# Optimization experiments

Hardware: AMD Instinct MI355X
Metric: run time of the kernel (lower is better)

The kernel has to match this reference:

```python
import jax, jax.numpy as jnp
import numpy as np
from jax import lax

H = 128      # hidden_size
KK = 4       # num_kernels (TemporalConv k)
NL = 2       # rgcn num_layers
C = 32       # convtranse channels
KS = 3       # convtranse kernel_size
NE = 40000   # num_ents
NR = 256     # num_rels
T = 4        # history length
E = 100000   # edges per snapshot
NT = 1024    # num query triplets


def _norm(x):
    return x / jnp.maximum(jnp.linalg.norm(x, axis=-1, keepdims=True), 1e-12)


def _gru(x, h, wih, whh, bih, bhh):
    gi = x @ wih.T + bih
    gh = h @ whh.T + bhh
    ir, iz, inn = jnp.split(gi, 3, axis=-1)
    hr, hz, hn = jnp.split(gh, 3, axis=-1)
    r = jax.nn.sigmoid(ir + hr)
    z = jax.nn.sigmoid(iz + hz)
    n = jnp.tanh(inn + r * hn)
    return (1.0 - z) * n + z * h


def _tconv(e, t, w, b, pw, pb):
    # e: (N,H), t: (1,H) -> kernels (KK,1,H//KK)
    v = (t @ w.T + b).reshape(KK, 1, -1)
    f = lax.conv_general_dilated(e[:, None, :], v, (1,), 'VALID',
                                 dimension_numbers=('NCH', 'OIH', 'NCH'))  # (N,KK,H-H//KK+1)
    return f.reshape(f.shape[0], -1) @ pw.T + pb


def _convtranse(x, ck, cb, fw, fb):
    p = KS // 2
    y = lax.conv_general_dilated(x, ck, (1,), [(p, p)],
                                 dimension_numbers=('NCH', 'OIH', 'NCH')) + cb[None, :, None]
    y = jax.nn.relu(y)
    return jax.nn.relu(y.reshape(y.shape[0], -1) @ fw.T + fb)


def _agg_rel(nf, s, d, r):
    # dense (num_rels, num_nodes) bool mask via scatter, then per-rel mean of touched nodes
    mask = jnp.zeros((NR, NE), bool).at[r, s].set(True).at[r, d].set(True)
    m = mask.astype(nf.dtype)
    su = m @ nf
    c = m.sum(1, keepdims=True)
    return jnp.where(c > 0, su / jnp.maximum(c, 1.0), 0.0)


def _rgcn(h, ef, s, d, wn, ws, b):
    ones = jnp.ones((s.shape[0], 1), h.dtype)
    for l in range(NL):
        msg = h[s] + ef
        sums = jax.ops.segment_sum(msg, d, num_segments=NE)
        cnt = jax.ops.segment_sum(ones, d, num_segments=NE)
        agg = sums / jnp.maximum(cnt, 1.0)
        h = jax.nn.relu(agg @ wn[l] + h @ ws[l] + b[l])
    return h


def setup_inputs() -> dict:
    key = jax.random.key(0)
    ks = jax.random.split(key, 40)
    f32 = jnp.float32
    pin = H * KK - H + KK  # TemporalConv pooling in-features
    inp = {
        'ent_embeds': jax.random.normal(ks[0], (NE, H), f32),
        'rel_embeds': jax.random.normal(ks[1], (NR, H), f32) * 0.1,
        'mmt_embed': jax.random.normal(ks[2], (1, H), f32) * 0.1,
        'tc_w': jax.random.normal(ks[3], (H, H), f32) * 0.05,
        'tc_b': jnp.zeros((H,), f32),
        'tc_pw': jax.random.normal(ks[4], (H, pin), f32) * 0.05,
        'tc_pb': jnp.zeros((H,), f32),
        'gru1_wih': jax.random.normal(ks[5], (3 * H, 2 * H), f32) * 0.05,
        'gru1_whh': jax.random.normal(ks[6], (3 * H, H), f32) * 0.05,
        'gru1_bih': jnp.zeros((3 * H,), f32),
        'gru1_bhh': jnp.zeros((3 * H,), f32),
        'l1_wih': jax.random.normal(ks[7], (3 * H, H), f32) * 0.05,
        'l1_whh': jax.random.normal(ks[8], (3 * H, H), f32) * 0.05,
        'l1_bih': jnp.zeros((3 * H,), f32),
        'l1_bhh': jnp.zeros((3 * H,), f32),
        'l2_wih': jax.random.normal(ks[9], (3 * H, H), f32) * 0.05,
        'l2_whh': jax.random.normal(ks[10], (3 * H, H), f32) * 0.05,
        'l2_bih': jnp.zeros((3 * H,), f32),
        'l2_bhh': jnp.zeros((3 * H,), f32),
        'lin_w': jax.random.normal(ks[11], (H, H), f32) * 0.05,
        'lin_b': jnp.zeros((H,), f32),
        'rgcn_wn': jax.random.normal(ks[12], (NL, H, H), f32) * 0.05,
        'rgcn_ws': jax.random.normal(ks[13], (NL, H, H), f32) * 0.05,
        'rgcn_b': jnp.zeros((NL, H), f32),
        'oc_k': jax.random.normal(ks[14], (C, 2, KS), f32) * 0.1,
        'oc_kb': jnp.zeros((C,), f32),
        'oc_fw': jax.random.normal(ks[15], (H, C * H), f32) * 0.02,
        'oc_fb': jnp.zeros((H,), f32),
        'rc_k': jax.random.normal(ks[16], (C, 2, KS), f32) * 0.1,
        'rc_kb': jnp.zeros((C,), f32),
        'rc_fw': jax.random.normal(ks[17], (H, C * H), f32) * 0.02,
        'rc_fb': jnp.zeros((H,), f32),
        'src': jax.random.randint(ks[18], (T, E), 0, NE, jnp.int32),
        'dst': jax.random.randint(ks[19], (T, E), 0, NE, jnp.int32),
        'rid': jax.random.randint(ks[20], (T, E), 0, NR, jnp.int32),
        'subj': jax.random.randint(ks[21], (NT,), 0, NE, jnp.int32),
        'rel': jax.random.randint(ks[22], (NT,), 0, NR, jnp.int32),
        'obj': jax.random.randint(ks[23], (NT,), 0, NE, jnp.int32),
    }
    return inp


def reference(ent_embeds, rel_embeds, mmt_embed, tc_w, tc_b, tc_pw, tc_pb,
              gru1_wih, gru1_whh, gru1_bih, gru1_bhh,
              l1_wih, l1_whh, l1_bih, l1_bhh,
              l2_wih, l2_whh, l2_bih, l2_bhh,
              lin_w, lin_b, rgcn_wn, rgcn_ws, rgcn_b,
              oc_k, oc_kb, oc_fw, oc_fb, rc_k, rc_kb, rc_fw, rc_fb,
              src, dst, rid, subj, rel, obj):
    rel_param = rel_embeds  # the raw parameter, used inside the loop
    ent = _norm(ent_embeds)
    relh = _norm(rel_embeds)
    mmt = mmt_embed
    zero = jnp.zeros_like(mmt)
    for t in range(T):
        s, d, r = src[t], dst[t], rid[t]
        n_mmt = _gru(mmt, zero, l1_wih, l1_whh, l1_bih, l1_bhh)
        g = _gru(mmt, zero, l2_wih, l2_whh, l2_bih, l2_bhh)
        mmt = mmt + g * (n_mmt - mmt)
        ent = _tconv(ent, mmt, tc_w, tc_b, tc_pw, tc_pb)
        relh = _tconv(relh, mmt, tc_w, tc_b, tc_pw, tc_pb)
        rel_ent = _agg_rel(ent, s, d, r)
        gru_in = jnp.concatenate([rel_ent, rel_param], axis=-1)
        n_rel = _gru(gru_in, relh, gru1_wih, gru1_whh, gru1_bih, gru1_bhh)
        n_rel = _norm(n_rel)
        efeat = n_rel[r]
        nf = _rgcn(ent, efeat, s, d, rgcn_wn, rgcn_ws, rgcn_b)
        nf = _norm(nf)
        u = jax.nn.sigmoid(ent @ lin_w.T + lin_b)
        ent = ent + u * (nf - ent)
        relh = n_rel
    obj_pred = jnp.stack([ent[subj], relh[rel]], axis=1)    # (NT,2,H)
    obj_logit = _convtranse(obj_pred, oc_k, oc_kb, oc_fw, oc_fb) @ ent.T
    rel_pred = jnp.stack([ent[subj], ent[obj]], axis=1)
    rel_logit = _convtranse(rel_pred, rc_k, rc_kb, rc_fw, rc_fb) @ relh.T
    return obj_logit, rel_logit
```

## Files before the change

kernel.cpp:

```cpp
#include <hip/hip_runtime.h>
#include <cmath>


namespace {

constexpr int H   = 128;
constexpr int KK  = 4;
constexpr int C   = 32;
constexpr int NE  = 40000;
constexpr int NR  = 256;
constexpr int T   = 4;
constexpr int E   = 100000;
constexpr int NT  = 1024;
constexpr int PIN = 388;
constexpr int MW  = 1280;
constexpr int MWU = 1250;
constexpr size_t NEH = (size_t)NE * H;

__device__ __forceinline__ float sigm(float x) { return 1.0f / (1.0f + expf(-x)); }

__global__ __launch_bounds__(256) void norm_rows(const float* __restrict__ in,
                                                 float* __restrict__ out, int n) {
  int row  = blockIdx.x * 4 + (threadIdx.x >> 6);
  int lane = threadIdx.x & 63;
  if (row >= n) return;
  const float2* ip = reinterpret_cast<const float2*>(in + (size_t)row * H);
  float2 v = ip[lane];
  float ss = v.x * v.x + v.y * v.y;
#pragma unroll
  for (int off = 32; off; off >>= 1) ss += __shfl_xor(ss, off);
  float inv = 1.0f / fmaxf(sqrtf(ss), 1e-12f);
  float2 o; o.x = v.x * inv; o.y = v.y * inv;
  reinterpret_cast<float2*>(out + (size_t)row * H)[lane] = o;
}

__global__ void copy_vec(const float* __restrict__ a, float* __restrict__ b, int n) {
  int i = blockIdx.x * blockDim.x + threadIdx.x;
  if (i < n) b[i] = a[i];
}

__global__ __launch_bounds__(256) void transpose128(const float* __restrict__ in,
                                                    float* __restrict__ out) {
  int i = blockIdx.x * 256 + threadIdx.x;
  int o = i >> 7, k = i & 127;
  out[k * H + o] = in[o * H + k];
}

__global__ __launch_bounds__(128) void mmt_step(
    const float* __restrict__ mmt_in,
    const float* __restrict__ w1, const float* __restrict__ bi1, const float* __restrict__ bh1,
    const float* __restrict__ w2, const float* __restrict__ bi2, const float* __restrict__ bh2,
    const float* __restrict__ tcw, const float* __restrict__ tcb,
    float* __restrict__ mmt_out, float* __restrict__ vout) {
  __shared__ float sm[H], sm2[H];
  int t = threadIdx.x;
  sm[t] = mmt_in[t];
  __syncthreads();
  float g1r = bi1[t], g1z = bi1[H + t], g1n = bi1[2 * H + t];
  float g2r = bi2[t], g2z = bi2[H + t], g2n = bi2[2 * H + t];
  for (int k = 0; k < H; k++) {
    float x = sm[k];
    g1r += x * w1[t * H + k];
    g1z += x * w1[(H + t) * H + k];
    g1n += x * w1[(2 * H + t) * H + k];
    g2r += x * w2[t * H + k];
    g2z += x * w2[(H + t) * H + k];
    g2n += x * w2[(2 * H + t) * H + k];
  }
  float r1 = sigm(g1r + bh1[t]), z1 = sigm(g1z + bh1[H + t]);
  float n1 = tanhf(g1n + r1 * bh1[2 * H + t]);
  float nmmt = (1.0f - z1) * n1;
  float r2 = sigm(g2r + bh2[t]), z2 = sigm(g2z + bh2[H + t]);
  float n2 = tanhf(g2n + r2 * bh2[2 * H + t]);
  float gg = (1.0f - z2) * n2;
  float m  = sm[t];
  float mo = m + gg * (nmmt - m);
  mmt_out[t] = mo;
  sm2[t] = mo;
  __syncthreads();
  float v = tcb[t];
  for (int k = 0; k < H; k++) v += sm2[k] * tcw[t * H + k];
  vout[t] = v;
}

__global__ __launch_bounds__(128) void build_M(const float* __restrict__ v,
                                               const float* __restrict__ pw,
                                               float* __restrict__ MT) {
  int o = blockIdx.x, p = threadIdx.x;
  __shared__ float sp[PIN];
  __shared__ float sv[H];
  for (int i = p; i < PIN; i += H) sp[i] = pw[(size_t)o * PIN + i];
  sv[p] = v[p];
  __syncthreads();
  float acc = 0.0f;
  int jlo = p - 31 > 0 ? p - 31 : 0;
  int jhi = p < 96 ? p : 96;
#pragma unroll
  for (int k = 0; k < KK; k++)
    for (int j = jlo; j <= jhi; j++) acc += sp[k * 97 + j] * sv[k * 32 + (p - j)];
  MT[p * H + o] = acc;
}


__global__ __launch_bounds__(256) void gemm_bias(const float* __restrict__ X,
                                                 const float* __restrict__ WT,
                                                 const float* __restrict__ bias,
                                                 float* __restrict__ out) {
  __shared__ float sX[64 * H];
  int t = threadIdx.x;
  int base = blockIdx.x * 64;
  const float4* gx = reinterpret_cast<const float4*>(X + (size_t)base * H);
  float4* sx4 = reinterpret_cast<float4*>(sX);
#pragma unroll
  for (int i = 0; i < 8; i++) sx4[t + 256 * i] = gx[t + 256 * i];
  __syncthreads();
  int oq = (t & 31) * 4, ng = (t >> 5) * 8;
  float acc[8][4] = {};
  for (int k = 0; k < H; k += 4) {
    float4 w0 = *reinterpret_cast<const float4*>(&WT[(k + 0) * H + oq]);
    float4 w1 = *reinterpret_cast<const float4*>(&WT[(k + 1) * H + oq]);
    float4 w2 = *reinterpret_cast<const float4*>(&WT[(k + 2) * H + oq]);
    float4 w3 = *reinterpret_cast<const float4*>(&WT[(k + 3) * H + oq]);
#pragma unroll
    for (int m = 0; m < 8; m++) {
      float4 x = *reinterpret_cast<const float4*>(&sX[(ng + m) * H + k]);
      acc[m][0] += x.x * w0.x + x.y * w1.x + x.z * w2.x + x.w * w3.x;
      acc[m][1] += x.x * w0.y + x.y * w1.y + x.z * w2.y + x.w * w3.y;
      acc[m][2] += x.x * w0.z + x.y * w1.z + x.z * w2.z + x.w * w3.z;
      acc[m][3] += x.x * w0.w + x.y * w1.w + x.z * w2.w + x.w * w3.w;
    }
  }
  float4 b4 = *reinterpret_cast<const float4*>(&bias[oq]);
#pragma unroll
  for (int m = 0; m < 8; m++) {
    float4 o4 = {acc[m][0] + b4.x, acc[m][1] + b4.y, acc[m][2] + b4.z, acc[m][3] + b4.w};
    *reinterpret_cast<float4*>(&out[(size_t)(base + ng + m) * H + oq]) = o4;
  }
}

__global__ __launch_bounds__(256) void gemm_rgcn(const float* __restrict__ A,
                                                 const float* __restrict__ Hm,
                                                 const float* __restrict__ wn,
                                                 const float* __restrict__ ws,
                                                 const float* __restrict__ bias,
                                                 const int* __restrict__ deg,
                                                 float* __restrict__ out) {
  __shared__ float sA[32 * H];
  __shared__ float sH[32 * H];
  int t = threadIdx.x;
  int base = blockIdx.x * 32;
  const float4* ga = reinterpret_cast<const float4*>(A + (size_t)base * H);
  const float4* gh = reinterpret_cast<const float4*>(Hm + (size_t)base * H);
  float4* sa4 = reinterpret_cast<float4*>(sA);
  float4* sh4 = reinterpret_cast<float4*>(sH);
#pragma unroll
  for (int i = 0; i < 4; i++) { sa4[t + 256 * i] = ga[t + 256 * i]; sh4[t + 256 * i] = gh[t + 256 * i]; }
  __syncthreads();
  int oq = (t & 31) * 4, ng = (t >> 5) * 4;
  float accA[4][4] = {}, accS[4][4] = {};
  for (int k = 0; k < H; k += 4) {
    float4 n0 = *reinterpret_cast<const float4*>(&wn[(k + 0) * H + oq]);
    float4 n1 = *reinterpret_cast<const float4*>(&wn[(k + 1) * H + oq]);
    float4 n2 = *reinterpret_cast<const float4*>(&wn[(k + 2) * H + oq]);
    float4 n3 = *reinterpret_cast<const float4*>(&wn[(k + 3) * H + oq]);
    float4 s0 = *reinterpret_cast<const float4*>(&ws[(k + 0) * H + oq]);
    float4 s1 = *reinterpret_cast<const float4*>(&ws[(k + 1) * H + oq]);
    float4 s2 = *reinterpret_cast<const float4*>(&ws[(k + 2) * H + oq]);
    float4 s3 = *reinterpret_cast<const float4*>(&ws[(k + 3) * H + oq]);
#pragma unroll
    for (int m = 0; m < 4; m++) {
      float4 a = *reinterpret_cast<const float4*>(&sA[(ng + m) * H + k]);
      float4 h = *reinterpret_cast<const float4*>(&sH[(ng + m) * H + k]);
      accA[m][0] += a.x * n0.x + a.y * n1.x + a.z * n2.x + a.w * n3.x;
      accA[m][1] += a.x * n0.y + a.y * n1.y + a.z * n2.y + a.w * n3.y;
      accA[m][2] += a.x * n0.z + a.y * n1.z + a.z * n2.z + a.w * n3.z;
      accA[m][3] += a.x * n0.w + a.y * n1.w + a.z * n2.w + a.w * n3.w;
      accS[m][0] += h.x * s0.x + h.y * s1.x + h.z * s2.x + h.w * s3.x;
      accS[m][1] += h.x * s0.y + h.y * s1.y + h.z * s2.y + h.w * s3.y;
      accS[m][2] += h.x * s0.z + h.y * s1.z + h.z * s2.z + h.w * s3.z;
      accS[m][3] += h.x * s0.w + h.y * s1.w + h.z * s2.w + h.w * s3.w;
    }
  }
  float4 b4 = *reinterpret_cast<const float4*>(&bias[oq]);
#pragma unroll
  for (int m = 0; m < 4; m++) {
    float inv = 1.0f / fmaxf((float)deg[base + ng + m], 1.0f);
    float4 o4 = {fmaxf(accA[m][0] * inv + accS[m][0] + b4.x, 0.0f),
                 fmaxf(accA[m][1] * inv + accS[m][1] + b4.y, 0.0f),
                 fmaxf(accA[m][2] * inv + accS[m][2] + b4.z, 0.0f),
                 fmaxf(accA[m][3] * inv + accS[m][3] + b4.w, 0.0f)};
    *reinterpret_cast<float4*>(&out[(size_t)(base + ng + m) * H + oq]) = o4;
  }
}

__global__ __launch_bounds__(256) void gemm_update(const float* __restrict__ Xe,
                                                   const float* __restrict__ WT,
                                                   const float* __restrict__ bias,
                                                   const float* __restrict__ nf,
                                                   float* __restrict__ out) {
  __shared__ float sX[64 * H];
  int t = threadIdx.x;
  int base = blockIdx.x * 64;
  const float4* gx = reinterpret_cast<const float4*>(Xe + (size_t)base * H);
  float4* sx4 = reinterpret_cast<float4*>(sX);
#pragma unroll
  for (int i = 0; i < 8; i++) sx4[t + 256 * i] = gx[t + 256 * i];
  __syncthreads();
  int oq = (t & 31) * 4, ng = (t >> 5) * 8;
  float acc[8][4] = {};
  for (int k = 0; k < H; k += 4) {
    float4 w0 = *reinterpret_cast<const float4*>(&WT[(k + 0) * H + oq]);
    float4 w1 = *reinterpret_cast<const float4*>(&WT[(k + 1) * H + oq]);
    float4 w2 = *reinterpret_cast<const float4*>(&WT[(k + 2) * H + oq]);
    float4 w3 = *reinterpret_cast<const float4*>(&WT[(k + 3) * H + oq]);
#pragma unroll
    for (int m = 0; m < 8; m++) {
      float4 x = *reinterpret_cast<const float4*>(&sX[(ng + m) * H + k]);
      acc[m][0] += x.x * w0.x + x.y * w1.x + x.z * w2.x + x.w * w3.x;
      acc[m][1] += x.x * w0.y + x.y * w1.y + x.z * w2.y + x.w * w3.y;
      acc[m][2] += x.x * w0.z + x.y * w1.z + x.z * w2.z + x.w * w3.z;
      acc[m][3] += x.x * w0.w + x.y * w1.w + x.z * w2.w + x.w * w3.w;
    }
  }
  float4 b4 = *reinterpret_cast<const float4*>(&bias[oq]);
#pragma unroll
  for (int m = 0; m < 8; m++) {
    size_t row = (size_t)(base + ng + m) * H;
    float4 e4 = *reinterpret_cast<const float4*>(&sX[(ng + m) * H + oq]);
    float4 f4 = *reinterpret_cast<const float4*>(&nf[row + oq]);
    float4 o4 = {e4.x + sigm(acc[m][0] + b4.x) * (f4.x - e4.x),
                 e4.y + sigm(acc[m][1] + b4.y) * (f4.y - e4.y),
                 e4.z + sigm(acc[m][2] + b4.z) * (f4.z - e4.z),
                 e4.w + sigm(acc[m][3] + b4.w) * (f4.w - e4.w)};
    *reinterpret_cast<float4*>(&out[row + oq]) = o4;
  }
}

__global__ __launch_bounds__(256) void edge_hist(const int* __restrict__ d, int* __restrict__ deg) {
  int e = blockIdx.x * 256 + threadIdx.x;
  if (e < E) atomicAdd(&deg[d[e]], 1);
}

__global__ __launch_bounds__(1024) void scan_deg(const int* __restrict__ deg,
                                                 int* __restrict__ rowptr,
                                                 int* __restrict__ wpos) {
  __shared__ int buf[1024];
  __shared__ int carry;
  int tid = threadIdx.x;
  if (tid == 0) carry = 0;
  __syncthreads();
  for (int base = 0; base < NE; base += 1024) {
    int idx = base + tid;
    int v = idx < NE ? deg[idx] : 0;
    buf[tid] = v;
    __syncthreads();
    for (int off = 1; off < 1024; off <<= 1) {
      int x = tid >= off ? buf[tid - off] : 0;
      __syncthreads();
      buf[tid] += x;
      __syncthreads();
    }
    int excl = carry + buf[tid] - v;
    int total = buf[1023];
    if (idx < NE) { rowptr[idx] = excl; wpos[idx] = excl; }
    __syncthreads();
    if (tid == 0) carry += total;
    __syncthreads();
  }
  if (tid == 0) rowptr[NE] = carry;
}

__global__ __launch_bounds__(256) void edge_fill(const int* __restrict__ d,
                                                 int* __restrict__ wpos,
                                                 int* __restrict__ elist) {
  int e = blockIdx.x * 256 + threadIdx.x;
  if (e >= E) return;
  int p = atomicAdd(&wpos[d[e]], 1);
  elist[p] = e;
}

__global__ __launch_bounds__(256) void rgcn_gather(const float* __restrict__ h,
                                                   const float* __restrict__ ef,
                                                   const int* __restrict__ rowptr,
                                                   const int* __restrict__ elist,
                                                   const int* __restrict__ s,
                                                   const int* __restrict__ r,
                                                   float* __restrict__ agg) {
  int node = blockIdx.x * 2 + (threadIdx.x >> 7);
  int dim  = threadIdx.x & 127;
  int b = rowptr[node], e2 = rowptr[node + 1];
  float acc = 0.0f;
  for (int i = b; i < e2; i++) {
    int e = elist[i];
    acc += h[(size_t)s[e] * H + dim] + ef[(size_t)r[e] * H + dim];
  }
  agg[(size_t)node * H + dim] = acc;
}

__global__ __launch_bounds__(256) void mask_scatter(const int* __restrict__ s,
                                                    const int* __restrict__ d,
                                                    const int* __restrict__ r,
                                                    unsigned int* __restrict__ mask) {
  int e = blockIdx.x * 256 + threadIdx.x;
  if (e >= E) return;
  int ri = r[e], si = s[e], di = d[e];
  atomicOr(&mask[(size_t)ri * MW + (si >> 5)], 1u << (si & 31));
  atomicOr(&mask[(size_t)ri * MW + (di >> 5)], 1u << (di & 31));
}

__global__ __launch_bounds__(128) void agg_rel_sum(const unsigned int* __restrict__ mask,
                                                   const float* __restrict__ ent,
                                                   float* __restrict__ rsum,
                                                   float* __restrict__ rcnt) {
  int rel = blockIdx.x, part = blockIdx.y, tid = threadIdx.x;
  const int WPS = (MWU + 7) / 8;
  int w0 = part * WPS;
  int w1 = w0 + WPS < MWU ? w0 + WPS : MWU;
  float acc = 0.0f, cnt = 0.0f;
  const unsigned int* mrow = mask + (size_t)rel * MW;
  for (int w = w0; w < w1; w++) {
    unsigned int bits = mrow[w];
    if (!bits) continue;
    cnt += (float)__popc(bits);
    int base = w << 5;
    while (bits) {
      int b = __ffs(bits) - 1;
      bits &= bits - 1;
      acc += ent[(size_t)(base + b) * H + tid];
    }
  }
  atomicAdd(&rsum[rel * H + tid], acc);
  if (tid == 0) atomicAdd(&rcnt[rel], cnt);
}

__global__ __launch_bounds__(128) void rel_gru(const float* __restrict__ rsum,
                                               const float* __restrict__ rcnt,
                                               const float* __restrict__ rel_param,
                                               const float* __restrict__ relh,
                                               const float* __restrict__ wih,
                                               const float* __restrict__ whh,
                                               const float* __restrict__ bih,
                                               const float* __restrict__ bhh,
                                               float* __restrict__ outp) {
  int rel = blockIdx.x, tid = threadIdx.x;
  __shared__ float sx[2 * H], sh[H], red[H];
  float c = rcnt[rel];
  sx[tid]     = c > 0.0f ? rsum[rel * H + tid] / fmaxf(c, 1.0f) : 0.0f;
  sx[H + tid] = rel_param[rel * H + tid];
  sh[tid]     = relh[rel * H + tid];
  __syncthreads();
  float gr = bih[tid], gz = bih[H + tid], gn = bih[2 * H + tid];
  for (int k = 0; k < 2 * H; k++) {
    float x = sx[k];
    gr += x * wih[(size_t)tid * 2 * H + k];
    gz += x * wih[(size_t)(H + tid) * 2 * H + k];
    gn += x * wih[(size_t)(2 * H + tid) * 2 * H + k];
  }
  float hr = bhh[tid], hz = bhh[H + tid], hn = bhh[2 * H + tid];
  for (int k = 0; k < H; k++) {
    float hv = sh[k];
    hr += hv * whh[tid * H + k];
    hz += hv * whh[(H + tid) * H + k];
    hn += hv * whh[(2 * H + tid) * H + k];
  }
  float r = sigm(gr + hr), z = sigm(gz + hz), nn = tanhf(gn + r * hn);
  float val = (1.0f - z) * nn + z * sh[tid];
  red[tid] = val * val;
  __syncthreads();
  for (int s2 = 64; s2 > 0; s2 >>= 1) {
    if (tid < s2) red[tid] += red[tid + s2];
    __syncthreads();
  }
  float inv = 1.0f / fmaxf(sqrtf(red[0]), 1e-12f);
  outp[rel * H + tid] = val * inv;
}

__global__ __launch_bounds__(256) void conv_front(const float* __restrict__ fa,
                                                  const int* __restrict__ ia,
                                                  const float* __restrict__ fbm,
                                                  const int* __restrict__ ib,
                                                  const float* __restrict__ ck,
                                                  const float* __restrict__ ckb,
                                                  const float* __restrict__ fw,
                                                  const float* __restrict__ fbias,
                                                  float* __restrict__ Z) {
  __shared__ float sy[4 * C * H];
  int q0 = blockIdx.x * 4;
  int tid = threadIdx.x;
  for (int i = tid; i < 4 * C * H; i += 256) {
    int q = i >> 12, c = (i >> 7) & 31, p = i & 127;
    const float* xa = fa + (size_t)ia[q0 + q] * H;
    const float* xb = fbm + (size_t)ib[q0 + q] * H;
    float acc = ckb[c];
#pragma unroll
    for (int kk2 = 0; kk2 < 3; kk2++) {
      int pos = p + kk2 - 1;
      if (pos >= 0 && pos < H)
        acc += xa[pos] * ck[c * 6 + kk2] + xb[pos] * ck[c * 6 + 3 + kk2];
    }
    sy[i] = fmaxf(acc, 0.0f);
  }
  __syncthreads();
  int o = tid & 127, g = tid >> 7;
  float acc0 = fbias[o], acc1 = fbias[o];
  const float* wrow = fw + (size_t)o * (C * H);
  const float* y0 = &sy[(g * 2 + 0) * C * H];
  const float* y1 = &sy[(g * 2 + 1) * C * H];
  for (int j = 0; j < C * H; j += 4) {
    float4 w = *reinterpret_cast<const float4*>(&wrow[j]);
    float4 a = *reinterpret_cast<const float4*>(&y0[j]);
    float4 b = *reinterpret_cast<const float4*>(&y1[j]);
    acc0 += a.x * w.x + a.y * w.y + a.z * w.z + a.w * w.w;
    acc1 += b.x * w.x + b.y * w.y + b.z * w.z + b.w * w.w;
  }
  Z[(size_t)(q0 + g * 2 + 0) * H + o] = fmaxf(acc0, 0.0f);
  Z[(size_t)(q0 + g * 2 + 1) * H + o] = fmaxf(acc1, 0.0f);
}

__global__ __launch_bounds__(256) void logits_gemm2(const float* __restrict__ Z,
                                                    const float* __restrict__ F,
                                                    float* __restrict__ out,
                                                    int M) {
  __shared__ float sZ[32 * H];
  __shared__ float sF[32 * H];
  int t = threadIdx.x;
  int bq = blockIdx.y * 128, bm = blockIdx.x * 128;
  int tx = t & 15, ty = t >> 4;
  float acc[8][8] = {};
  int qld = t & 127, kh = (t >> 7) * 16;
  int mld = bm + qld;
  if (mld >= M) mld = M - 1;
  for (int kc = 0; kc < H; kc += 32) {
    __syncthreads();
    const float* zr = Z + (size_t)(bq + qld) * H + kc + kh;
    const float* fr = F + (size_t)mld * H + kc + kh;
#pragma unroll
    for (int j = 0; j < 16; j += 4) {
      float4 v = *reinterpret_cast<const float4*>(zr + j);
      sZ[(kh + j + 0) * H + qld] = v.x;
      sZ[(kh + j + 1) * H + qld] = v.y;
      sZ[(kh + j + 2) * H + qld] = v.z;
      sZ[(kh + j + 3) * H + qld] = v.w;
      float4 f = *reinterpret_cast<const float4*>(fr + j);
      sF[(kh + j + 0) * H + qld] = f.x;
      sF[(kh + j + 1) * H + qld] = f.y;
      sF[(kh + j + 2) * H + qld] = f.z;
      sF[(kh + j + 3) * H + qld] = f.w;
    }
    __syncthreads();
    for (int k = 0; k < 32; k++) {
      float4 za = *reinterpret_cast<const float4*>(&sZ[k * H + ty * 8]);
      float4 zb = *reinterpret_cast<const float4*>(&sZ[k * H + ty * 8 + 4]);
      float4 fa = *reinterpret_cast<const float4*>(&sF[k * H + tx * 8]);
      float4 fb = *reinterpret_cast<const float4*>(&sF[k * H + tx * 8 + 4]);
      float zq[8] = {za.x, za.y, za.z, za.w, zb.x, zb.y, zb.z, zb.w};
      float fm[8] = {fa.x, fa.y, fa.z, fa.w, fb.x, fb.y, fb.z, fb.w};
#pragma unroll
      for (int i = 0; i < 8; i++)
#pragma unroll
        for (int j = 0; j < 8; j++) acc[i][j] += zq[i] * fm[j];
    }
  }
  int m0 = bm + tx * 8;
  if (m0 >= M) return;
#pragma unroll
  for (int i = 0; i < 8; i++) {
    size_t row = (size_t)(bq + ty * 8 + i) * (size_t)M + m0;
    float4 o1 = {acc[i][0], acc[i][1], acc[i][2], acc[i][3]};
    float4 o2 = {acc[i][4], acc[i][5], acc[i][6], acc[i][7]};
    *reinterpret_cast<float4*>(&out[row]) = o1;
    *reinterpret_cast<float4*>(&out[row + 4]) = o2;
  }
}

}

extern "C" void kernel_launch(void* const* d_in, const int* in_sizes, int n_in,
                              void* d_out, int out_size, void* d_ws, size_t ws_size,
                              hipStream_t stream) {
  (void)in_sizes; (void)n_in; (void)out_size; (void)ws_size;
  const float* ent_embeds = (const float*)d_in[0];
  const float* rel_embeds = (const float*)d_in[1];
  const float* mmt_embed  = (const float*)d_in[2];
  const float* tc_w  = (const float*)d_in[3];
  const float* tc_b  = (const float*)d_in[4];
  const float* tc_pw = (const float*)d_in[5];
  const float* tc_pb = (const float*)d_in[6];
  const float* g1_wih = (const float*)d_in[7];
  const float* g1_whh = (const float*)d_in[8];
  const float* g1_bih = (const float*)d_in[9];
  const float* g1_bhh = (const float*)d_in[10];
  const float* l1_wih = (const float*)d_in[11];
  const float* l1_bih = (const float*)d_in[13];
  const float* l1_bhh = (const float*)d_in[14];
  const float* l2_wih = (const float*)d_in[15];
  const float* l2_bih = (const float*)d_in[17];
  const float* l2_bhh = (const float*)d_in[18];
  const float* lin_w = (const float*)d_in[19];
  const float* lin_b = (const float*)d_in[20];
  const float* rgcn_wn = (const float*)d_in[21];
  const float* rgcn_ws = (const float*)d_in[22];
  const float* rgcn_b  = (const float*)d_in[23];
  const float* oc_k  = (const float*)d_in[24];
  const float* oc_kb = (const float*)d_in[25];
  const float* oc_fw = (const float*)d_in[26];
  const float* oc_fb = (const float*)d_in[27];
  const float* rc_k  = (const float*)d_in[28];
  const float* rc_kb = (const float*)d_in[29];
  const float* rc_fw = (const float*)d_in[30];
  const float* rc_fb = (const float*)d_in[31];
  const int* src  = (const int*)d_in[32];
  const int* dst  = (const int*)d_in[33];
  const int* rid  = (const int*)d_in[34];
  const int* qsub = (const int*)d_in[35];
  const int* qrel = (const int*)d_in[36];
  const int* qobj = (const int*)d_in[37];

  float* out = (float*)d_out;
  float* ws  = (float*)d_ws;

  size_t off = 0;
  float* entF = ws + off; off += NEH;
  float* relhB[3] = {ws + off, ws + off + (size_t)NR * H, ws + off + 2 * (size_t)NR * H};
  off += 3 * (size_t)NR * H;
  float* rel_sum = ws + off; off += (size_t)NR * H;
  float* rcnt    = ws + off; off += NR;
  float* mmtbuf0 = ws + off; off += H;
  float* mmtbuf1 = ws + off; off += H;
  float* vbuf    = ws + off; off += H;
  float* MT      = ws + off; off += (size_t)H * H;
  float* WTlin   = ws + off; off += (size_t)H * H;
  float* Zo      = ws + off; off += (size_t)NT * H;
  float* Zr      = ws + off; off += (size_t)NT * H;
  unsigned int* mask = (unsigned int*)(ws + off); off += (size_t)NR * MW;

  float* B[4] = {out, out + NEH, out + 2 * NEH, out + 3 * NEH};
  int* itail   = (int*)(out + 4 * NEH);
  int* deg     = itail;
  int* rowptr  = itail + NE;
  int* wpos    = itail + 2 * NE + 1;
  int* elist   = itail + 3 * NE + 1;
  float* mmtb[2] = {mmtbuf0, mmtbuf1};

  norm_rows<<<(NE + 3) / 4, 256, 0, stream>>>(ent_embeds, B[0], NE);
  norm_rows<<<(NR + 3) / 4, 256, 0, stream>>>(rel_embeds, relhB[0], NR);
  copy_vec<<<1, 128, 0, stream>>>(mmt_embed, mmtbuf0, H);
  transpose128<<<64, 256, 0, stream>>>(lin_w, WTlin);

  int cur = 0, curRelh = 0;
  for (int t = 0; t < T; t++) {
    int fr[3], fi = 0;
    for (int b = 0; b < 4; b++) if (b != cur) fr[fi++] = b;
    int bX = fr[0], bG = fr[1], bY = fr[2];
    const int* s_t = src + (size_t)t * E;
    const int* d_t = dst + (size_t)t * E;
    const int* r_t = rid + (size_t)t * E;

    mmt_step<<<1, 128, 0, stream>>>(mmtb[t & 1], l1_wih, l1_bih, l1_bhh,
                                    l2_wih, l2_bih, l2_bhh, tc_w, tc_b,
                                    mmtb[(t + 1) & 1], vbuf);
    build_M<<<H, H, 0, stream>>>(vbuf, tc_pw, MT);
    gemm_bias<<<NE / 64, 256, 0, stream>>>(B[cur], MT, tc_pb, B[bX]);
    gemm_bias<<<NR / 64, 256, 0, stream>>>(relhB[curRelh], MT, tc_pb, relhB[2]);

    hipMemsetAsync(mask, 0, (size_t)NR * MW * 4, stream);
    mask_scatter<<<(E + 255) / 256, 256, 0, stream>>>(s_t, d_t, r_t, mask);
    hipMemsetAsync(rel_sum, 0, ((size_t)NR * H + NR) * 4, stream);
    agg_rel_sum<<<dim3(NR, 8), 128, 0, stream>>>(mask, B[bX], rel_sum, rcnt);
    int nextRelh = 1 - curRelh;
    rel_gru<<<NR, 128, 0, stream>>>(rel_sum, rcnt, rel_embeds, relhB[2],
                                    g1_wih, g1_whh, g1_bih, g1_bhh, relhB[nextRelh]);

    hipMemsetAsync(deg, 0, (size_t)NE * 4, stream);
    edge_hist<<<(E + 255) / 256, 256, 0, stream>>>(d_t, deg);
    scan_deg<<<1, 1024, 0, stream>>>(deg, rowptr, wpos);
    edge_fill<<<(E + 255) / 256, 256, 0, stream>>>(d_t, wpos, elist);

    rgcn_gather<<<NE / 2, 256, 0, stream>>>(B[bX], relhB[nextRelh], rowptr, elist, s_t, r_t, B[bG]);
    gemm_rgcn<<<NE / 32, 256, 0, stream>>>(B[bG], B[bX], rgcn_wn, rgcn_ws, rgcn_b, deg, B[bY]);
    rgcn_gather<<<NE / 2, 256, 0, stream>>>(B[bY], relhB[nextRelh], rowptr, elist, s_t, r_t, B[bG]);
    gemm_rgcn<<<NE / 32, 256, 0, stream>>>(B[bG], B[bY], rgcn_wn + H * H, rgcn_ws + H * H,
                                           rgcn_b + H, deg, B[cur]);

    norm_rows<<<NE / 4, 256, 0, stream>>>(B[cur], B[cur], NE);
    float* entDst = (t == T - 1) ? entF : B[bY];
    gemm_update<<<NE / 64, 256, 0, stream>>>(B[bX], WTlin, lin_b, B[cur], entDst);

    cur = bY;
    curRelh = nextRelh;
  }

  float* relhF = relhB[curRelh];

  conv_front<<<NT / 4, 256, 0, stream>>>(entF, qsub, relhF, qrel, oc_k, oc_kb, oc_fw, oc_fb, Zo);
  conv_front<<<NT / 4, 256, 0, stream>>>(entF, qsub, entF, qobj, rc_k, rc_kb, rc_fw, rc_fb, Zr);

  logits_gemm2<<<dim3((NE + 127) / 128, NT / 128), 256, 0, stream>>>(Zo, entF, out, NE);
  logits_gemm2<<<dim3(NR / 128, NT / 128), 256, 0, stream>>>(Zr, relhF, out + (size_t)NT * NE, NR);
}
```

Before: 2.527 ms.

## Fuse edge prep and row norm, split convtranse over channels, vectorize GRU matvecs

Several independent changes. The mask scatter and degree histogram now run as one edge kernel. The L2 row normalisation is folded into the second RGCN GEMM epilogue using a wavefront shuffle reduction. The degree scan uses wave shuffles instead of a barrier-heavy shared-memory scan. agg_rel_sum gets more partitions and skips zero atomics. The conv_front kernel is split across 4 channel groups, with partial sums reduced in a new finalize kernel, to raise parallelism. The GRU and mmt matvecs now read weights as float4. Risks are the extra finalize launches and partial buffers, plus more atomics in agg_rel_sum.

Measured after the change: 2.305 ms. 1.1x faster.

```diff
diff --git a/kernel.cpp b/kernel.cpp
--- a/kernel.cpp
+++ b/kernel.cpp
@@ -58,14 +58,24 @@
   __syncthreads();
   float g1r = bi1[t], g1z = bi1[H + t], g1n = bi1[2 * H + t];
   float g2r = bi2[t], g2z = bi2[H + t], g2n = bi2[2 * H + t];
-  for (int k = 0; k < H; k++) {
-    float x = sm[k];
-    g1r += x * w1[t * H + k];
-    g1z += x * w1[(H + t) * H + k];
-    g1n += x * w1[(2 * H + t) * H + k];
-    g2r += x * w2[t * H + k];
-    g2z += x * w2[(H + t) * H + k];
-    g2n += x * w2[(2 * H + t) * H + k];
+  {
+    const float4* r1p = reinterpret_cast<const float4*>(w1 + (size_t)t * H);
+    const float4* z1p = reinterpret_cast<const float4*>(w1 + (size_t)(H + t) * H);
+    const float4* n1p = reinterpret_cast<const float4*>(w1 + (size_t)(2 * H + t) * H);
+    const float4* r2p = reinterpret_cast<const float4*>(w2 + (size_t)t * H);
+    const float4* z2p = reinterpret_cast<const float4*>(w2 + (size_t)(H + t) * H);
+    const float4* n2p = reinterpret_cast<const float4*>(w2 + (size_t)(2 * H + t) * H);
+    const float4* x4 = reinterpret_cast<const float4*>(sm);
+    for (int k = 0; k < 32; k++) {
+      float4 x = x4[k];
+      float4 a = r1p[k], b = z1p[k], c = n1p[k], d = r2p[k], e = z2p[k], f = n2p[k];
+      g1r += x.x * a.x + x.y * a.y + x.z * a.z + x.w * a.w;
+      g1z += x.x * b.x + x.y * b.y + x.z * b.z + x.w * b.w;
+      g1n += x.x * c.x + x.y * c.y + x.z * c.z + x.w * c.w;
+      g2r += x.x * d.x + x.y * d.y + x.z * d.z + x.w * d.w;
+      g2z += x.x * e.x + x.y * e.y + x.z * e.z + x.w * e.w;
+      g2n += x.x * f.x + x.y * f.y + x.z * f.z + x.w * f.w;
+    }
   }
   float r1 = sigm(g1r + bh1[t]), z1 = sigm(g1z + bh1[H + t]);
   float n1 = tanhf(g1n + r1 * bh1[2 * H + t]);
@@ -79,7 +89,14 @@
   sm2[t] = mo;
   __syncthreads();
   float v = tcb[t];
-  for (int k = 0; k < H; k++) v += sm2[k] * tcw[t * H + k];
+  {
+    const float4* wp = reinterpret_cast<const float4*>(tcw + (size_t)t * H);
+    const float4* x4 = reinterpret_cast<const float4*>(sm2);
+    for (int k = 0; k < 32; k++) {
+      float4 x = x4[k], w = wp[k];
+      v += x.x * w.x + x.y * w.y + x.z * w.z + x.w * w.w;
+    }
+  }
   vout[t] = v;
 }
 
@@ -100,7 +117,6 @@
     for (int j = jlo; j <= jhi; j++) acc += sp[k * 97 + j] * sv[k * 32 + (p - j)];
   MT[p * H + o] = acc;
 }
-
 
 __global__ __launch_bounds__(256) void gemm_bias(const float* __restrict__ X,
                                                  const float* __restrict__ WT,
@@ -144,7 +160,8 @@
                                                  const float* __restrict__ ws,
                                                  const float* __restrict__ bias,
                                                  const int* __restrict__ deg,
-                                                 float* __restrict__ out) {
+                                                 float* __restrict__ out,
+                                                 int donorm) {
   __shared__ float sA[32 * H];
   __shared__ float sH[32 * H];
   int t = threadIdx.x;
@@ -182,13 +199,28 @@
     }
   }
   float4 b4 = *reinterpret_cast<const float4*>(&bias[oq]);
+  float v[4][4];
 #pragma unroll
   for (int m = 0; m < 4; m++) {
     float inv = 1.0f / fmaxf((float)deg[base + ng + m], 1.0f);
-    float4 o4 = {fmaxf(accA[m][0] * inv + accS[m][0] + b4.x, 0.0f),
-                 fmaxf(accA[m][1] * inv + accS[m][1] + b4.y, 0.0f),
-                 fmaxf(accA[m][2] * inv + accS[m][2] + b4.z, 0.0f),
-                 fmaxf(accA[m][3] * inv + accS[m][3] + b4.w, 0.0f)};
+    v[m][0] = fmaxf(accA[m][0] * inv + accS[m][0] + b4.x, 0.0f);
+    v[m][1] = fmaxf(accA[m][1] * inv + accS[m][1] + b4.y, 0.0f);
+    v[m][2] = fmaxf(accA[m][2] * inv + accS[m][2] + b4.z, 0.0f);
+    v[m][3] = fmaxf(accA[m][3] * inv + accS[m][3] + b4.w, 0.0f);
+  }
+  if (donorm) {
+#pragma unroll
+    for (int m = 0; m < 4; m++) {
+      float ss = v[m][0]*v[m][0] + v[m][1]*v[m][1] + v[m][2]*v[m][2] + v[m][3]*v[m][3];
+#pragma unroll
+      for (int off = 16; off; off >>= 1) ss += __shfl_xor(ss, off);
+      float inv = 1.0f / fmaxf(sqrtf(ss), 1e-12f);
+      v[m][0] *= inv; v[m][1] *= inv; v[m][2] *= inv; v[m][3] *= inv;
+    }
+  }
+#pragma unroll
+  for (int m = 0; m < 4; m++) {
+    float4 o4 = {v[m][0], v[m][1], v[m][2], v[m][3]};
     *reinterpret_cast<float4*>(&out[(size_t)(base + ng + m) * H + oq]) = o4;
   }
 }
@@ -236,38 +268,48 @@
   }
 }
 
-__global__ __launch_bounds__(256) void edge_hist(const int* __restrict__ d, int* __restrict__ deg) {
+__global__ __launch_bounds__(256) void edge_prep(const int* __restrict__ s,
+                                                 const int* __restrict__ d,
+                                                 const int* __restrict__ r,
+                                                 unsigned int* __restrict__ mask,
+                                                 int* __restrict__ deg) {
   int e = blockIdx.x * 256 + threadIdx.x;
-  if (e < E) atomicAdd(&deg[d[e]], 1);
+  if (e >= E) return;
+  int ri = r[e], si = s[e], di = d[e];
+  atomicOr(&mask[(size_t)ri * MW + (si >> 5)], 1u << (si & 31));
+  atomicOr(&mask[(size_t)ri * MW + (di >> 5)], 1u << (di & 31));
+  atomicAdd(&deg[di], 1);
 }
 
 __global__ __launch_bounds__(1024) void scan_deg(const int* __restrict__ deg,
                                                  int* __restrict__ rowptr,
                                                  int* __restrict__ wpos) {
-  __shared__ int buf[1024];
-  __shared__ int carry;
-  int tid = threadIdx.x;
-  if (tid == 0) carry = 0;
+  __shared__ int wsum[16];
+  __shared__ int carry_s;
+  int tid = threadIdx.x, lane = tid & 63, w = tid >> 6;
+  if (tid == 0) carry_s = 0;
   __syncthreads();
   for (int base = 0; base < NE; base += 1024) {
     int idx = base + tid;
     int v = idx < NE ? deg[idx] : 0;
-    buf[tid] = v;
+    int x = v;
+#pragma unroll
+    for (int off = 1; off < 64; off <<= 1) {
+      int y = __shfl_up(x, off, 64);
+      if (lane >= off) x += y;
+    }
+    if (lane == 63) wsum[w] = x;
     __syncthreads();
-    for (int off = 1; off < 1024; off <<= 1) {
-      int x = tid >= off ? buf[tid - off] : 0;
-      __syncthreads();
-      buf[tid] += x;
-      __syncthreads();
-    }
-    int excl = carry + buf[tid] - v;
-    int total = buf[1023];
+    int carry = carry_s;
+    int wpre = 0;
+    for (int i = 0; i < w; i++) wpre += wsum[i];
+    int excl = carry + wpre + x - v;
     if (idx < NE) { rowptr[idx] = excl; wpos[idx] = excl; }
     __syncthreads();
-    if (tid == 0) carry += total;
-    __syncthreads();
-  }
-  if (tid == 0) rowptr[NE] = carry;
+    if (tid == 1023) carry_s = carry + wpre + x;
+  }
+  __syncthreads();
+  if (tid == 0) rowptr[NE] = carry_s;
 }
 
 __global__ __launch_bounds__(256) void edge_fill(const int* __restrict__ d,
@@ -297,23 +339,12 @@
   agg[(size_t)node * H + dim] = acc;
 }
 
-__global__ __launch_bounds__(256) void mask_scatter(const int* __restrict__ s,
-                                                    const int* __restrict__ d,
-                                                    const int* __restrict__ r,
-                                                    unsigned int* __restrict__ mask) {
-  int e = blockIdx.x * 256 + threadIdx.x;
-  if (e >= E) return;
-  int ri = r[e], si = s[e], di = d[e];
-  atomicOr(&mask[(size_t)ri * MW + (si >> 5)], 1u << (si & 31));
-  atomicOr(&mask[(size_t)ri * MW + (di >> 5)], 1u << (di & 31));
-}
-
 __global__ __launch_bounds__(128) void agg_rel_sum(const unsigned int* __restrict__ mask,
                                                    const float* __restrict__ ent,
                                                    float* __restrict__ rsum,
                                                    float* __restrict__ rcnt) {
   int rel = blockIdx.x, part = blockIdx.y, tid = threadIdx.x;
-  const int WPS = (MWU + 7) / 8;
+  const int WPS = (MWU + 31) / 32;
   int w0 = part * WPS;
   int w1 = w0 + WPS < MWU ? w0 + WPS : MWU;
   float acc = 0.0f, cnt = 0.0f;
@@ -329,8 +360,8 @@
       acc += ent[(size_t)(base + b) * H + tid];
     }
   }
-  atomicAdd(&rsum[rel * H + tid], acc);
-  if (tid == 0) atomicAdd(&rcnt[rel], cnt);
+  if (acc != 0.0f) atomicAdd(&rsum[rel * H + tid], acc);
+  if (tid == 0 && cnt != 0.0f) atomicAdd(&rcnt[rel], cnt);
 }
 
 __global__ __launch_bounds__(128) void rel_gru(const float* __restrict__ rsum,
@@ -350,18 +381,32 @@
   sh[tid]     = relh[rel * H + tid];
   __syncthreads();
   float gr = bih[tid], gz = bih[H + tid], gn = bih[2 * H + tid];
-  for (int k = 0; k < 2 * H; k++) {
-    float x = sx[k];
-    gr += x * wih[(size_t)tid * 2 * H + k];
-    gz += x * wih[(size_t)(H + tid) * 2 * H + k];
-    gn += x * wih[(size_t)(2 * H + tid) * 2 * H + k];
+  {
+    const float4* rp = reinterpret_cast<const float4*>(wih + (size_t)tid * 2 * H);
+    const float4* zp = reinterpret_cast<const float4*>(wih + (size_t)(H + tid) * 2 * H);
+    const float4* np = reinterpret_cast<const float4*>(wih + (size_t)(2 * H + tid) * 2 * H);
+    const float4* x4 = reinterpret_cast<const float4*>(sx);
+    for (int k = 0; k < 64; k++) {
+      float4 x = x4[k];
+      float4 a = rp[k], b = zp[k], cc = np[k];
+      gr += x.x * a.x + x.y * a.y + x.z * a.z + x.w * a.w;
+      gz += x.x * b.x + x.y * b.y + x.z * b.z + x.w * b.w;
+      gn += x.x * cc.x + x.y * cc.y + x.z * cc.z + x.w * cc.w;
+    }
   }
   float hr = bhh[tid], hz = bhh[H + tid], hn = bhh[2 * H + tid];
-  for (int k = 0; k < H; k++) {
-    float hv = sh[k];
-    hr += hv * whh[tid * H + k];
-    hz += hv * whh[(H + tid) * H + k];
-    hn += hv * whh[(2 * H + tid) * H + k];
+  {
+    const float4* rp = reinterpret_cast<const float4*>(whh + (size_t)tid * H);
+    const float4* zp = reinterpret_cast<const float4*>(whh + (size_t)(H + tid) * H);
+    const float4* np = reinterpret_cast<const float4*>(whh + (size_t)(2 * H + tid) * H);
+    const float4* h4 = reinterpret_cast<const float4*>(sh);
+    for (int k = 0; k < 32; k++) {
+      float4 x = h4[k];
+      float4 a = rp[k], b = zp[k], cc = np[k];
+      hr += x.x * a.x + x.y * a.y + x.z * a.z + x.w * a.w;
+      hz += x.x * b.x + x.y * b.y + x.z * b.z + x.w * b.w;
+      hn += x.x * cc.x + x.y * cc.y + x.z * cc.z + x.w * cc.w;
+    }
   }
   float r = sigm(gr + hr), z = sigm(gz + hz), nn = tanhf(gn + r * hn);
   float val = (1.0f - z) * nn + z * sh[tid];
@@ -382,39 +427,67 @@
                                                   const float* __restrict__ ck,
                                                   const float* __restrict__ ckb,
                                                   const float* __restrict__ fw,
-                                                  const float* __restrict__ fbias,
-                                                  float* __restrict__ Z) {
-  __shared__ float sy[4 * C * H];
-  int q0 = blockIdx.x * 4;
+                                                  float* __restrict__ Zp) {
+  __shared__ float sx[8 * 2 * H];
+  __shared__ float sy[8 * 1024];
+  __shared__ float sck[48];
+  __shared__ float sckb[8];
   int tid = threadIdx.x;
-  for (int i = tid; i < 4 * C * H; i += 256) {
-    int q = i >> 12, c = (i >> 7) & 31, p = i & 127;
-    const float* xa = fa + (size_t)ia[q0 + q] * H;
-    const float* xb = fbm + (size_t)ib[q0 + q] * H;
-    float acc = ckb[c];
-#pragma unroll
-    for (int kk2 = 0; kk2 < 3; kk2++) {
-      int pos = p + kk2 - 1;
+  int q0 = blockIdx.x * 8, ks = blockIdx.y;
+  if (tid < 48) sck[tid] = ck[ks * 48 + tid];
+  if (tid < 8)  sckb[tid] = ckb[ks * 8 + tid];
+#pragma unroll
+  for (int i = tid; i < 2048; i += 256) {
+    int q = i >> 8, half = (i >> 7) & 1, p = i & 127;
+    int node = (half ? ib : ia)[q0 + q];
+    const float* srcp = (half ? fbm : fa) + (size_t)node * H + p;
+    sx[i] = *srcp;
+  }
+  __syncthreads();
+#pragma unroll
+  for (int i = tid; i < 8192; i += 256) {
+    int q = i >> 10, c = (i >> 7) & 7, p = i & 127;
+    const float* xq = &sx[q * 256];
+    float acc = sckb[c];
+#pragma unroll
+    for (int kk = 0; kk < 3; kk++) {
+      int pos = p + kk - 1;
       if (pos >= 0 && pos < H)
-        acc += xa[pos] * ck[c * 6 + kk2] + xb[pos] * ck[c * 6 + 3 + kk2];
+        acc += xq[pos] * sck[c * 6 + kk] + xq[128 + pos] * sck[c * 6 + 3 + kk];
     }
     sy[i] = fmaxf(acc, 0.0f);
   }
   __syncthreads();
-  int o = tid & 127, g = tid >> 7;
-  float acc0 = fbias[o], acc1 = fbias[o];
-  const float* wrow = fw + (size_t)o * (C * H);
-  const float* y0 = &sy[(g * 2 + 0) * C * H];
-  const float* y1 = &sy[(g * 2 + 1) * C * H];
-  for (int j = 0; j < C * H; j += 4) {
-    float4 w = *reinterpret_cast<const float4*>(&wrow[j]);
-    float4 a = *reinterpret_cast<const float4*>(&y0[j]);
-    float4 b = *reinterpret_cast<const float4*>(&y1[j]);
-    acc0 += a.x * w.x + a.y * w.y + a.z * w.z + a.w * w.w;
-    acc1 += b.x * w.x + b.y * w.y + b.z * w.z + b.w * w.w;
-  }
-  Z[(size_t)(q0 + g * 2 + 0) * H + o] = fmaxf(acc0, 0.0f);
-  Z[(size_t)(q0 + g * 2 + 1) * H + o] = fmaxf(acc1, 0.0f);
+  int ot = tid & 63, qg = tid >> 6;
+  const float* w0p = fw + (size_t)ot * 4096 + ks * 1024;
+  const float* w1p = fw + (size_t)(ot + 64) * 4096 + ks * 1024;
+  const float* y0p = &sy[(qg * 2 + 0) * 1024];
+  const float* y1p = &sy[(qg * 2 + 1) * 1024];
+  float a00 = 0, a01 = 0, a10 = 0, a11 = 0;
+  for (int j = 0; j < 1024; j += 4) {
+    float4 w0 = *reinterpret_cast<const float4*>(w0p + j);
+    float4 w1 = *reinterpret_cast<const float4*>(w1p + j);
+    float4 y0 = *reinterpret_cast<const float4*>(y0p + j);
+    float4 y1 = *reinterpret_cast<const float4*>(y1p + j);
+    a00 += y0.x * w0.x + y0.y * w0.y + y0.z * w0.z + y0.w * w0.w;
+    a10 += y0.x * w1.x + y0.y * w1.y + y0.z * w1.z + y0.w * w1.w;
+    a01 += y1.x * w0.x + y1.y * w0.y + y1.z * w0.z + y1.w * w0.w;
+    a11 += y1.x * w1.x + y1.y * w1.y + y1.z * w1.z + y1.w * w1.w;
+  }
+  float* zb = Zp + (size_t)ks * NT * H;
+  zb[(size_t)(q0 + qg * 2 + 0) * H + ot]      = a00;
+  zb[(size_t)(q0 + qg * 2 + 0) * H + ot + 64] = a10;
+  zb[(size_t)(q0 + qg * 2 + 1) * H + ot]      = a01;
+  zb[(size_t)(q0 + qg * 2 + 1) * H + ot + 64] = a11;
+}
+
+__global__ __launch_bounds__(256) void conv_finalize(const float* __restrict__ Zp,
+                                                     const float* __restrict__ fb,
+                                                     float* __restrict__ Z) {
+  int i = blockIdx.x * 256 + threadIdx.x;
+  int o = i & 127;
+  float v = Zp[i] + Zp[NT * H + i] + Zp[2 * NT * H + i] + Zp[3 * NT * H + i] + fb[o];
+  Z[i] = fmaxf(v, 0.0f);
 }
 
 __global__ __launch_bounds__(256) void logits_gemm2(const float* __restrict__ Z,
@@ -452,9 +525,9 @@
       float4 za = *reinterpret_cast<const float4*>(&sZ[k * H + ty * 8]);
       float4 zb = *reinterpret_cast<const float4*>(&sZ[k * H + ty * 8 + 4]);
       float4 fa = *reinterpret_cast<const float4*>(&sF[k * H + tx * 8]);
-      float4 fb = *reinterpret_cast<const float4*>(&sF[k * H + tx * 8 + 4]);
+      float4 fbv = *reinterpret_cast<const float4*>(&sF[k * H + tx * 8 + 4]);
       float zq[8] = {za.x, za.y, za.z, za.w, zb.x, zb.y, zb.z, zb.w};
-      float fm[8] = {fa.x, fa.y, fa.z, fa.w, fb.x, fb.y, fb.z, fb.w};
+      float fm[8] = {fa.x, fa.y, fa.z, fa.w, fbv.x, fbv.y, fbv.z, fbv.w};
 #pragma unroll
       for (int i = 0; i < 8; i++)
 #pragma unroll
@@ -532,6 +605,7 @@
   float* WTlin   = ws + off; off += (size_t)H * H;
   float* Zo      = ws + off; off += (size_t)NT * H;
   float* Zr      = ws + off; off += (size_t)NT * H;
+  float* Zpart   = ws + off; off += 4 * (size_t)NT * H;
   unsigned int* mask = (unsigned int*)(ws + off); off += (size_t)NR * MW;
 
   float* B[4] = {out, out + NEH, out + 2 * NEH, out + 3 * NEH};
@@ -564,25 +638,24 @@
     gemm_bias<<<NR / 64, 256, 0, stream>>>(relhB[curRelh], MT, tc_pb, relhB[2]);
 
     hipMemsetAsync(mask, 0, (size_t)NR * MW * 4, stream);
-    mask_scatter<<<(E + 255) / 256, 256, 0, stream>>>(s_t, d_t, r_t, mask);
+    hipMemsetAsync(deg, 0, (size_t)NE * 4, stream);
+    edge_prep<<<(E + 255) / 256, 256, 0, stream>>>(s_t, d_t, r_t, mask, deg);
+
     hipMemsetAsync(rel_sum, 0, ((size_t)NR * H + NR) * 4, stream);
-    agg_rel_sum<<<dim3(NR, 8), 128, 0, stream>>>(mask, B[bX], rel_sum, rcnt);
+    agg_rel_sum<<<dim3(NR, 32), 128, 0, stream>>>(mask, B[bX], rel_sum, rcnt);
     int nextRelh = 1 - curRelh;
     rel_gru<<<NR, 128, 0, stream>>>(rel_sum, rcnt, rel_embeds, relhB[2],
                                     g1_wih, g1_whh, g1_bih, g1_bhh, relhB[nextRelh]);
 
-    hipMemsetAsync(deg, 0, (size_t)NE * 4, stream);
-    edge_hist<<<(E + 255) / 256, 256, 0, stream>>>(d_t, deg);
     scan_deg<<<1, 1024, 0, stream>>>(deg, rowptr, wpos);
     edge_fill<<<(E + 255) / 256, 256, 0, stream>>>(d_t, wpos, elist);
 
     rgcn_gather<<<NE / 2, 256, 0, stream>>>(B[bX], relhB[nextRelh], rowptr, elist, s_t, r_t, B[bG]);
-    gemm_rgcn<<<NE / 32, 256, 0, stream>>>(B[bG], B[bX], rgcn_wn, rgcn_ws, rgcn_b, deg, B[bY]);
+    gemm_rgcn<<<NE / 32, 256, 0, stream>>>(B[bG], B[bX], rgcn_wn, rgcn_ws, rgcn_b, deg, B[bY], 0);
     rgcn_gather<<<NE / 2, 256, 0, stream>>>(B[bY], relhB[nextRelh], rowptr, elist, s_t, r_t, B[bG]);
     gemm_rgcn<<<NE / 32, 256, 0, stream>>>(B[bG], B[bY], rgcn_wn + H * H, rgcn_ws + H * H,
-                                           rgcn_b + H, deg, B[cur]);
-
-    norm_rows<<<NE / 4, 256, 0, stream>>>(B[cur], B[cur], NE);
+                                           rgcn_b + H, deg, B[cur], 1);
+
     float* entDst = (t == T - 1) ? entF : B[bY];
     gemm_update<<<NE / 64, 256, 0, stream>>>(B[bX], WTlin, lin_b, B[cur], entDst);
 
@@ -592,8 +665,10 @@
 
   float* relhF = relhB[curRelh];
 
-  conv_front<<<NT / 4, 256, 0, stream>>>(entF, qsub, relhF, qrel, oc_k, oc_kb, oc_fw, oc_fb, Zo);
-  conv_front<<<NT / 4, 256, 0, stream>>>(entF, qsub, entF, qobj, rc_k, rc_kb, rc_fw, rc_fb, Zr);
+  conv_front<<<dim3(NT / 8, 4), 256, 0, stream>>>(entF, qsub, relhF, qrel, oc_k, oc_kb, oc_fw, Zpart);
+  conv_finalize<<<NT * H / 256, 256, 0, stream>>>(Zpart, oc_fb, Zo);
+  conv_front<<<dim3(NT / 8, 4), 256, 0, stream>>>(entF, qsub, entF, qobj, rc_k, rc_kb, rc_fw, Zpart);
+  conv_finalize<<<NT * H / 256, 256, 0, stream>>>(Zpart, rc_fb, Zr);
 
   logits_gemm2<<<dim3((NE + 127) / 128, NT / 128), 256, 0, stream>>>(Zo, entF, out, NE);
   logits_gemm2<<<dim3(NR / 128, NT / 128), 256, 0, stream>>>(Zr, relhF, out + (size_t)NT * NE, NR);
```
